# Performance work log

Measured on AMD Instinct MI355X. Metric: run time of the kernel, lower is better.

## Reference

```python
import jax, jax.numpy as jnp
import numpy as np

N = 200000          # nodes
E = 6400000         # edges
F_IN, F_HID, F_OUT = 256, 16, 3
BN_EPS = 1e-5


def setup_inputs() -> dict:
    key = jax.random.key(0)
    ks = jax.random.split(key, 8)
    x = jax.random.normal(ks[0], (N, F_IN), dtype=jnp.float32)
    edge_index = jax.random.randint(ks[1], (2, E), 0, N, dtype=jnp.int64)
    # GCNConv params (PyG: glorot weight, zero bias)
    W1 = jax.random.normal(ks[2], (F_IN, F_HID), dtype=jnp.float32) * (1.0 / np.sqrt(F_IN))
    b1 = jnp.zeros((F_HID,), dtype=jnp.float32)
    W2 = jax.random.normal(ks[3], (F_HID, F_OUT), dtype=jnp.float32) * (1.0 / np.sqrt(F_HID))
    b2 = jnp.zeros((F_OUT,), dtype=jnp.float32)
    # BatchNorm1d affine params
    gamma = jnp.ones((F_HID,), dtype=jnp.float32)
    beta = jnp.zeros((F_HID,), dtype=jnp.float32)
    return {"x": x, "W1": W1, "b1": b1, "gamma": gamma, "beta": beta,
            "W2": W2, "b2": b2, "edge_index": edge_index}


def reference(x, W1, b1, gamma, beta, W2, b2, edge_index):
    n = x.shape[0]
    self_loop = jnp.arange(n, dtype=edge_index.dtype)
    src = jnp.concatenate([edge_index[0], self_loop])  # [E+N]
    dst = jnp.concatenate([edge_index[1], self_loop])
    # symmetric normalization D^{-1/2} (A+I) D^{-1/2}
    deg = jax.ops.segment_sum(jnp.ones_like(dst, dtype=x.dtype), dst, num_segments=n)
    dinv = jax.lax.rsqrt(deg)  # deg >= 1 due to self-loops
    ew = (dinv[src] * dinv[dst])[:, None]  # [E+N, 1]

    def gcn_conv(h, W, b):
        m = h @ W                                    # transform first (small out dim)
        agg = jax.ops.segment_sum(m[src] * ew, dst, num_segments=n)
        return agg + b

    h = gcn_conv(x, W1, b1)                          # [N, 16]
    # BatchNorm1d (training-mode batch statistics, biased variance)
    mu = h.mean(axis=0)
    var = h.var(axis=0)
    h = (h - mu) * jax.lax.rsqrt(var + BN_EPS) * gamma + beta
    h = jax.nn.relu(h)
    out = gcn_conv(h, W2, b2)                        # [N, 3]
    return jax.nn.log_softmax(out, axis=1)
```

## Files before the change

kernel.cpp:

```cpp
#include <hip/hip_runtime.h>
#include <math.h>

#define F_IN 256
#define F_HID 16
#define F_OUT 3
#define BN_EPS 1e-5f
#define CAP 72

#define BUCK_SHIFT 8
#define BUCK_NODES 256
#define MAXBUCK 1024
#define CAP2 9216
#define BIN_TPB 1024
#define BIN_EPT 16
#define BIN_CHUNK (BIN_TPB * BIN_EPT)

typedef float f32x4 __attribute__((ext_vector_type(4)));
typedef short s16x8 __attribute__((ext_vector_type(8)));

__device__ __forceinline__ unsigned short bf16_rne(float f) {
    union { float f; unsigned int u; } v; v.f = f;
    unsigned int u = v.u;
    unsigned int r = (u + 0x7FFFu + ((u >> 16) & 1u)) >> 16;
    return (unsigned short)r;
}
__device__ __forceinline__ float bf16_to_f(unsigned short h) {
    union { unsigned int u; float f; } v; v.u = ((unsigned int)h) << 16;
    return v.f;
}
__device__ __forceinline__ float bflo(unsigned int w) {
    union { unsigned int u; float f; } v; v.u = w << 16; return v.f;
}
__device__ __forceinline__ float bfhi(unsigned int w) {
    union { unsigned int u; float f; } v; v.u = w & 0xFFFF0000u; return v.f;
}

__global__ void k_zero(int* __restrict__ p, int n) {
    int i = blockIdx.x * blockDim.x + threadIdx.x;
    if (i < n) p[i] = 0;
}

__global__ __launch_bounds__(BIN_TPB) void k_bin(const int* __restrict__ src,
        const int* __restrict__ dst, int* __restrict__ gcur,
        unsigned int* __restrict__ bins, int e, int nbuck) {
    __shared__ int hist[MAXBUCK];
    __shared__ int base[MAXBUCK];
    int tid = threadIdx.x;
    for (int b = tid; b < nbuck; b += BIN_TPB) hist[b] = 0;
    __syncthreads();
    int k0 = blockIdx.x * BIN_CHUNK;
    int myd[BIN_EPT], mys[BIN_EPT];
    #pragma unroll
    for (int j = 0; j < BIN_EPT; ++j) {
        int k = k0 + tid + j * BIN_TPB;
        if (k < e) {
            myd[j] = dst[k];
            mys[j] = src[k];
            atomicAdd(&hist[myd[j] >> BUCK_SHIFT], 1);
        } else {
            myd[j] = -1;
        }
    }
    __syncthreads();
    for (int b = tid; b < nbuck; b += BIN_TPB) {
        int c = hist[b];
        base[b] = (c > 0) ? atomicAdd(&gcur[b], c) : 0;
        hist[b] = 0;
    }
    __syncthreads();
    #pragma unroll
    for (int j = 0; j < BIN_EPT; ++j) {
        if (myd[j] >= 0) {
            int b = myd[j] >> BUCK_SHIFT;
            int p = atomicAdd(&hist[b], 1) + base[b];
            if (p < CAP2)
                bins[(size_t)b * CAP2 + p] =
                    ((unsigned int)mys[j] << BUCK_SHIFT) |
                    (unsigned int)(myd[j] & (BUCK_NODES - 1));
        }
    }
}

__global__ __launch_bounds__(1024) void k_regroup(const unsigned int* __restrict__ bins,
        const int* __restrict__ gcur, int* __restrict__ ssrcp,
        int* __restrict__ cnt, int n) {
    __shared__ int hist[BUCK_NODES];
    __shared__ int cur[BUCK_NODES];
    int b = blockIdx.x, tid = threadIdx.x;
    if (tid < BUCK_NODES) { hist[tid] = 0; cur[tid] = 0; }
    __syncthreads();
    int m = min(gcur[b], CAP2);
    const unsigned int* row = bins + (size_t)b * CAP2;
    for (int k = tid; k < m; k += 1024)
        atomicAdd(&hist[row[k] & (BUCK_NODES - 1)], 1);
    __syncthreads();
    if (tid < BUCK_NODES) {
        int node = b * BUCK_NODES + tid;
        if (node < n) cnt[node] = hist[tid];
    }
    for (int k = tid; k < m; k += 1024) {
        unsigned int w = row[k];
        int dl = (int)(w & (BUCK_NODES - 1));
        int p = atomicAdd(&cur[dl], 1);
        if (p < CAP)
            ssrcp[((size_t)b * BUCK_NODES + dl) * CAP + p] = (int)(w >> BUCK_SHIFT);
    }
}

__global__ __launch_bounds__(256) void k_gemm1m(
    const float* __restrict__ x, const float* __restrict__ W1,
    const int* __restrict__ cnt, unsigned int* __restrict__ msc2, int n) {
    __shared__ __align__(16) unsigned short wp[8][2][64][8];
    int tid = threadIdx.x;
    for (int idx = tid; idx < 4096; idx += 256) {
        int j = idx & 7, l = (idx >> 3) & 63, s = idx >> 9;
        int g = l >> 4, f = l & 15;
        int k = 32 * s + 4 * g + (j & 3) + ((j >> 2) << 4);
        float w = W1[k * F_HID + f];
        unsigned short hi = bf16_rne(w);
        unsigned short lo = bf16_rne(w - bf16_to_f(hi));
        wp[s][0][l][j] = hi;
        wp[s][1][l][j] = lo;
    }
    __syncthreads();
    int wid = tid >> 6, lane = tid & 63;
    int tile = blockIdx.x * 4 + wid;
    int n0 = tile * 16;
    if (n0 >= n) return;
    int g = lane >> 4, ar = lane & 15;
    const float* xr = x + (size_t)(n0 + ar) * F_IN;
    f32x4 acc = {0.f, 0.f, 0.f, 0.f};
    #pragma unroll
    for (int s = 0; s < 8; ++s) {
        float4 a0 = *(const float4*)(xr + 32 * s + 4 * g);
        float4 a1 = *(const float4*)(xr + 32 * s + 16 + 4 * g);
        float av[8] = {a0.x, a0.y, a0.z, a0.w, a1.x, a1.y, a1.z, a1.w};
        s16x8 vah, val;
        #pragma unroll
        for (int j = 0; j < 8; ++j) {
            unsigned short hi = bf16_rne(av[j]);
            unsigned short lo = bf16_rne(av[j] - bf16_to_f(hi));
            vah[j] = (short)hi;
            val[j] = (short)lo;
        }
        s16x8 bh = *(const s16x8*)&wp[s][0][lane][0];
        s16x8 bl = *(const s16x8*)&wp[s][1][lane][0];
        acc = __builtin_amdgcn_mfma_f32_16x16x32_bf16(val, bh, acc, 0, 0, 0);
        acc = __builtin_amdgcn_mfma_f32_16x16x32_bf16(vah, bl, acc, 0, 0, 0);
        acc = __builtin_amdgcn_mfma_f32_16x16x32_bf16(vah, bh, acc, 0, 0, 0);
    }
    int f = lane & 15;
    #pragma unroll
    for (int q = 0; q < 4; ++q) {
        int node = n0 + 4 * g + q;
        float di = (node < n) ? rsqrtf(1.f + (float)cnt[node]) : 0.f;
        float v = acc[q] * di;
        float vp = __shfl_xor(v, 1);
        if (((lane & 1) == 0) && node < n) {
            unsigned int pk = ((unsigned int)bf16_rne(vp) << 16) | (unsigned int)bf16_rne(v);
            msc2[(size_t)node * 8 + (f >> 1)] = pk;
        }
    }
}

__global__ __launch_bounds__(256) void k_agg1p(const unsigned int* __restrict__ msc2,
        const int* __restrict__ cnt, const int* __restrict__ ssrcp,
        const float* __restrict__ b1, float* __restrict__ h, int n) {
    int wave = (blockIdx.x * blockDim.x + threadIdx.x) >> 6;
    if (wave >= n) return;
    int lane = threadIdx.x & 63;
    int f2 = lane & 7, e8 = lane >> 3;
    int deg = cnt[wave];
    int m = min(deg, CAP);
    const int* row = ssrcp + (size_t)wave * CAP;
    int sidx[9];
    #pragma unroll
    for (int j = 0; j < 9; ++j) {
        int k = e8 + 8 * j;
        int rv = row[k];
        sidx[j] = (k < m) ? rv : wave;
    }
    unsigned int sw = msc2[(size_t)wave * 8 + f2];
    float a0 = (e8 == 0) ? bflo(sw) : 0.f;
    float a1 = (e8 == 0) ? bfhi(sw) : 0.f;
    #pragma unroll
    for (int j = 0; j < 9; ++j) {
        unsigned int w = msc2[(size_t)sidx[j] * 8 + f2];
        bool p = (e8 + 8 * j) < m;
        a0 += p ? bflo(w) : 0.f;
        a1 += p ? bfhi(w) : 0.f;
    }
    a0 += __shfl_xor(a0, 8);  a1 += __shfl_xor(a1, 8);
    a0 += __shfl_xor(a0, 16); a1 += __shfl_xor(a1, 16);
    a0 += __shfl_xor(a0, 32); a1 += __shfl_xor(a1, 32);
    if (e8 == 0) {
        float di = rsqrtf(1.f + (float)deg);
        float2 o = {di * a0 + b1[2 * f2], di * a1 + b1[2 * f2 + 1]};
        *(float2*)&h[(size_t)wave * F_HID + 2 * f2] = o;
    }
}

__global__ __launch_bounds__(256) void k_bnstats1(const float* __restrict__ h,
                                                  float* __restrict__ partial, int n) {
    __shared__ float lds[4][32];
    int i = blockIdx.x * 256 + threadIdx.x;
    float s[F_HID], s2[F_HID];
    #pragma unroll
    for (int j = 0; j < F_HID; ++j) { s[j] = 0.f; s2[j] = 0.f; }
    if (i < n) {
        const float4* a = (const float4*)(h + (size_t)i * F_HID);
        #pragma unroll
        for (int q = 0; q < 4; ++q) {
            float4 v = a[q];
            s[q*4+0] = v.x; s2[q*4+0] = v.x * v.x;
            s[q*4+1] = v.y; s2[q*4+1] = v.y * v.y;
            s[q*4+2] = v.z; s2[q*4+2] = v.z * v.z;
            s[q*4+3] = v.w; s2[q*4+3] = v.w * v.w;
        }
    }
    int lane = threadIdx.x & 63, w = threadIdx.x >> 6;
    #pragma unroll
    for (int j = 0; j < F_HID; ++j) {
        float v = s[j], u = s2[j];
        #pragma unroll
        for (int off = 32; off > 0; off >>= 1) {
            v += __shfl_xor(v, off);
            u += __shfl_xor(u, off);
        }
        if (lane == 0) { lds[w][j] = v; lds[w][F_HID + j] = u; }
    }
    __syncthreads();
    if (threadIdx.x < 32) {
        float t = lds[0][threadIdx.x] + lds[1][threadIdx.x]
                + lds[2][threadIdx.x] + lds[3][threadIdx.x];
        partial[(size_t)blockIdx.x * 32 + threadIdx.x] = t;
    }
}

__global__ __launch_bounds__(256) void k_bnstats2(const float* __restrict__ partial,
                                                  float* __restrict__ bnsum, int nb) {
    __shared__ float lds[8][32];
    int j = threadIdx.x & 31, c = threadIdx.x >> 5;
    float acc = 0.f;
    for (int b = c; b < nb; b += 8)
        acc += partial[(size_t)b * 32 + j];
    lds[c][j] = acc;
    __syncthreads();
    if (threadIdx.x < 32) {
        float t = 0.f;
        #pragma unroll
        for (int c2 = 0; c2 < 8; ++c2) t += lds[c2][threadIdx.x];
        bnsum[threadIdx.x] = t;
    }
}

__global__ void k_bn_gemm2p(const float* __restrict__ h, const int* __restrict__ cnt,
        const float* __restrict__ gamma, const float* __restrict__ beta,
        const float* __restrict__ bnsum, const float* __restrict__ W2,
        uint2* __restrict__ m2s2, int n) {
    int i = blockIdx.x * blockDim.x + threadIdx.x;
    if (i >= n) return;
    float inv_n = 1.0f / (float)n;
    float hb[F_HID];
    const float4* a = (const float4*)(h + (size_t)i * F_HID);
    #pragma unroll
    for (int q = 0; q < 4; ++q) {
        float4 v = a[q];
        float hv[4] = {v.x, v.y, v.z, v.w};
        #pragma unroll
        for (int u = 0; u < 4; ++u) {
            int j = q * 4 + u;
            float S = bnsum[j], S2 = bnsum[F_HID + j];
            float mu = S * inv_n;
            float var = fmaxf(S2 * inv_n - mu * mu, 0.f);
            float bn = (hv[u] - mu) * rsqrtf(var + BN_EPS) * gamma[j] + beta[j];
            hb[j] = fmaxf(bn, 0.f);
        }
    }
    float di = rsqrtf(1.f + (float)cnt[i]);
    float op[F_OUT];
    #pragma unroll
    for (int j = 0; j < F_OUT; ++j) {
        float acc = 0.f;
        #pragma unroll
        for (int k = 0; k < F_HID; ++k)
            acc += hb[k] * W2[k * F_OUT + j];
        op[j] = acc * di;
    }
    uint2 pk;
    pk.x = ((unsigned int)bf16_rne(op[1]) << 16) | (unsigned int)bf16_rne(op[0]);
    pk.y = (unsigned int)bf16_rne(op[2]);
    m2s2[i] = pk;
}

__global__ __launch_bounds__(256) void k_agg2p(const unsigned short* __restrict__ m2,
        const int* __restrict__ cnt, const int* __restrict__ ssrcp,
        const float* __restrict__ b2, float* __restrict__ out, int n) {
    int wave = (blockIdx.x * blockDim.x + threadIdx.x) >> 6;
    if (wave >= n) return;
    int lane = threadIdx.x & 63;
    int f = lane & 3, e16 = lane >> 2;
    int deg = cnt[wave];
    int m = min(deg, CAP);
    const int* row = ssrcp + (size_t)wave * CAP;
    int sidx[5];
    #pragma unroll
    for (int j = 0; j < 5; ++j) {
        int k = e16 + 16 * j;
        int rv = row[min(k, CAP - 1)];
        sidx[j] = (k < m) ? rv : wave;
    }
    float self = bf16_to_f(m2[(size_t)wave * 4 + f]);
    float acc = (e16 == 0) ? self : 0.f;
    #pragma unroll
    for (int j = 0; j < 5; ++j) {
        float v = bf16_to_f(m2[(size_t)sidx[j] * 4 + f]);
        acc += ((e16 + 16 * j) < m) ? v : 0.f;
    }
    acc += __shfl_xor(acc, 4);
    acc += __shfl_xor(acc, 8);
    acc += __shfl_xor(acc, 16);
    acc += __shfl_xor(acc, 32);
    float o = rsqrtf(1.f + (float)deg) * acc + ((f < 3) ? b2[f] : -1e30f);
    int base = lane & ~3;
    float o0 = __shfl(o, base + 0);
    float o1 = __shfl(o, base + 1);
    float o2 = __shfl(o, base + 2);
    float mm = fmaxf(o0, fmaxf(o1, o2));
    float lse = mm + logf(expf(o0 - mm) + expf(o1 - mm) + expf(o2 - mm));
    if (f < 3) out[(size_t)wave * 3 + f] = o - lse;
}

__global__ void k_scatterpad(const int* __restrict__ src, const int* __restrict__ dst,
                             int* __restrict__ cnt, int* __restrict__ ssrcp, int e) {
    int i = blockIdx.x * blockDim.x + threadIdx.x;
    if (i >= e) return;
    int d = dst[i];
    int pos = atomicAdd(&cnt[d], 1);
    if (pos < CAP)
        __builtin_nontemporal_store(src[i], &ssrcp[(size_t)d * CAP + pos]);
}


extern "C" void kernel_launch(void* const* d_in, const int* in_sizes, int n_in,
                              void* d_out, int out_size, void* d_ws, size_t ws_size,
                              hipStream_t stream) {
    const float* x     = (const float*)d_in[0];
    const float* W1    = (const float*)d_in[1];
    const float* b1    = (const float*)d_in[2];
    const float* gamma = (const float*)d_in[3];
    const float* beta  = (const float*)d_in[4];
    const float* W2    = (const float*)d_in[5];
    const float* b2    = (const float*)d_in[6];
    const int*   ei    = (const int*)d_in[7];

    int n = in_sizes[0] / F_IN;
    int e = in_sizes[7] / 2;
    const int* srcIdx = ei;
    const int* dstIdx = ei + e;

    int nb    = (n + 255) / 256;
    int eb    = (e + 255) / 256;
    int mb    = (n + 63) / 64;
    int wb    = (n + 3) / 4;
    int nbuck = (n + BUCK_NODES - 1) / BUCK_NODES;
    int binb  = (e + BIN_CHUNK - 1) / BIN_CHUNK;

    size_t fcnt = (size_t)26 * n + 32 + (size_t)nb * 32;
    size_t bins_cnt = (size_t)nbuck * CAP2;
    size_t union_cnt = fcnt > bins_cnt ? fcnt : bins_cnt;
    size_t bucket_need = (union_cnt + (size_t)nbuck + (size_t)n + (size_t)n * CAP) * 4;

    float* fw      = (float*)d_ws;
    unsigned int* msc2 = (unsigned int*)fw;
    float* hbuf    = fw + (size_t)8 * n;
    uint2* m2s2    = (uint2*)(fw + (size_t)24 * n);
    float* bnsum   = fw + (size_t)26 * n;
    float* partial = fw + (size_t)26 * n + 32;
    unsigned int* bins = (unsigned int*)fw;
    int* iw    = (int*)(fw + union_cnt);
    int* gcur  = iw;
    int* cnt   = iw + nbuck;
    int* ssrcp = iw + nbuck + n;

    if (ws_size >= bucket_need) {
        k_zero     <<<1, 1024, 0, stream>>>(gcur, nbuck);
        k_bin      <<<binb, BIN_TPB, 0, stream>>>(srcIdx, dstIdx, gcur, bins, e, nbuck);
        k_regroup  <<<nbuck, 1024, 0, stream>>>(bins, gcur, ssrcp, cnt, n);
        k_gemm1m   <<<mb, 256, 0, stream>>>(x, W1, cnt, msc2, n);
        k_agg1p    <<<wb, 256, 0, stream>>>(msc2, cnt, ssrcp, b1, hbuf, n);
        k_bnstats1 <<<nb, 256, 0, stream>>>(hbuf, partial, n);
        k_bnstats2 <<<1, 256, 0, stream>>>(partial, bnsum, nb);
        k_bn_gemm2p<<<nb, 256, 0, stream>>>(hbuf, cnt, gamma, beta, bnsum, W2, m2s2, n);
        k_agg2p    <<<wb, 256, 0, stream>>>((const unsigned short*)m2s2, cnt, ssrcp, b2,
                                            (float*)d_out, n);
    } else {
        int* iw2    = (int*)(fw + fcnt);
        int* cnt2   = iw2;
        int* ssrcp2 = iw2 + n;
        k_zero      <<<nb, 256, 0, stream>>>(cnt2, n);
        k_scatterpad<<<eb, 256, 0, stream>>>(srcIdx, dstIdx, cnt2, ssrcp2, e);
        k_gemm1m    <<<mb, 256, 0, stream>>>(x, W1, cnt2, msc2, n);
        k_agg1p     <<<wb, 256, 0, stream>>>(msc2, cnt2, ssrcp2, b1, hbuf, n);
        k_bnstats1  <<<nb, 256, 0, stream>>>(hbuf, partial, n);
        k_bnstats2  <<<1, 256, 0, stream>>>(partial, bnsum, nb);
        k_bn_gemm2p <<<nb, 256, 0, stream>>>(hbuf, cnt2, gamma, beta, bnsum, W2, m2s2, n);
        k_agg2p     <<<wb, 256, 0, stream>>>((const unsigned short*)m2s2, cnt2, ssrcp2, b2,
                                             (float*)d_out, n);
    }
}
```

Before: 323.5 us.

## Split first-layer messages into two feature halves and drop low-bf16 x term

The bf16 messages from the first GEMM are stored as two separate 8-feature arrays, each 16 bytes per node, instead of one 32-byte-per-node array. Aggregation runs as two launches, one per half, so each pass gathers from a smaller array that fits caches better, at the cost of reading the neighbour index lists twice. The GEMM also drops the low-part correction MFMA for x (the x-lo × W-hi term), cutting one MFMA and the conversion work per step while slightly reducing precision.

After: 346.4 us. +7.1%, slower.

```diff
diff --git a/kernel.cpp b/kernel.cpp
--- a/kernel.cpp
+++ b/kernel.cpp
@@ -109,7 +109,8 @@
 
 __global__ __launch_bounds__(256) void k_gemm1m(
     const float* __restrict__ x, const float* __restrict__ W1,
-    const int* __restrict__ cnt, unsigned int* __restrict__ msc2, int n) {
+    const int* __restrict__ cnt, unsigned int* __restrict__ mscA,
+    unsigned int* __restrict__ mscB, int n) {
     __shared__ __align__(16) unsigned short wp[8][2][64][8];
     int tid = threadIdx.x;
     for (int idx = tid; idx < 4096; idx += 256) {
@@ -135,17 +136,12 @@
         float4 a0 = *(const float4*)(xr + 32 * s + 4 * g);
         float4 a1 = *(const float4*)(xr + 32 * s + 16 + 4 * g);
         float av[8] = {a0.x, a0.y, a0.z, a0.w, a1.x, a1.y, a1.z, a1.w};
-        s16x8 vah, val;
-        #pragma unroll
-        for (int j = 0; j < 8; ++j) {
-            unsigned short hi = bf16_rne(av[j]);
-            unsigned short lo = bf16_rne(av[j] - bf16_to_f(hi));
-            vah[j] = (short)hi;
-            val[j] = (short)lo;
-        }
+        s16x8 vah;
+        #pragma unroll
+        for (int j = 0; j < 8; ++j)
+            vah[j] = (short)bf16_rne(av[j]);
         s16x8 bh = *(const s16x8*)&wp[s][0][lane][0];
         s16x8 bl = *(const s16x8*)&wp[s][1][lane][0];
-        acc = __builtin_amdgcn_mfma_f32_16x16x32_bf16(val, bh, acc, 0, 0, 0);
         acc = __builtin_amdgcn_mfma_f32_16x16x32_bf16(vah, bl, acc, 0, 0, 0);
         acc = __builtin_amdgcn_mfma_f32_16x16x32_bf16(vah, bh, acc, 0, 0, 0);
     }
@@ -158,45 +154,47 @@
         float vp = __shfl_xor(v, 1);
         if (((lane & 1) == 0) && node < n) {
             unsigned int pk = ((unsigned int)bf16_rne(vp) << 16) | (unsigned int)bf16_rne(v);
-            msc2[(size_t)node * 8 + (f >> 1)] = pk;
-        }
-    }
-}
-
-__global__ __launch_bounds__(256) void k_agg1p(const unsigned int* __restrict__ msc2,
+            if (f < 8) mscA[(size_t)node * 4 + (f >> 1)] = pk;
+            else       mscB[(size_t)node * 4 + ((f - 8) >> 1)] = pk;
+        }
+    }
+}
+
+__global__ __launch_bounds__(256) void k_agg1h(const unsigned int* __restrict__ msch,
         const int* __restrict__ cnt, const int* __restrict__ ssrcp,
-        const float* __restrict__ b1, float* __restrict__ h, int n) {
+        const float* __restrict__ b1, float* __restrict__ h, int n, int foff) {
     int wave = (blockIdx.x * blockDim.x + threadIdx.x) >> 6;
     if (wave >= n) return;
     int lane = threadIdx.x & 63;
-    int f2 = lane & 7, e8 = lane >> 3;
+    int f4 = lane & 3, e16 = lane >> 2;
     int deg = cnt[wave];
     int m = min(deg, CAP);
     const int* row = ssrcp + (size_t)wave * CAP;
-    int sidx[9];
-    #pragma unroll
-    for (int j = 0; j < 9; ++j) {
-        int k = e8 + 8 * j;
-        int rv = row[k];
+    int sidx[5];
+    #pragma unroll
+    for (int j = 0; j < 5; ++j) {
+        int k = e16 + 16 * j;
+        int rv = row[min(k, CAP - 1)];
         sidx[j] = (k < m) ? rv : wave;
     }
-    unsigned int sw = msc2[(size_t)wave * 8 + f2];
-    float a0 = (e8 == 0) ? bflo(sw) : 0.f;
-    float a1 = (e8 == 0) ? bfhi(sw) : 0.f;
-    #pragma unroll
-    for (int j = 0; j < 9; ++j) {
-        unsigned int w = msc2[(size_t)sidx[j] * 8 + f2];
-        bool p = (e8 + 8 * j) < m;
+    unsigned int sw = msch[(size_t)wave * 4 + f4];
+    float a0 = (e16 == 0) ? bflo(sw) : 0.f;
+    float a1 = (e16 == 0) ? bfhi(sw) : 0.f;
+    #pragma unroll
+    for (int j = 0; j < 5; ++j) {
+        unsigned int w = msch[(size_t)sidx[j] * 4 + f4];
+        bool p = (e16 + 16 * j) < m;
         a0 += p ? bflo(w) : 0.f;
         a1 += p ? bfhi(w) : 0.f;
     }
+    a0 += __shfl_xor(a0, 4);  a1 += __shfl_xor(a1, 4);
     a0 += __shfl_xor(a0, 8);  a1 += __shfl_xor(a1, 8);
     a0 += __shfl_xor(a0, 16); a1 += __shfl_xor(a1, 16);
     a0 += __shfl_xor(a0, 32); a1 += __shfl_xor(a1, 32);
-    if (e8 == 0) {
+    if (e16 == 0) {
         float di = rsqrtf(1.f + (float)deg);
-        float2 o = {di * a0 + b1[2 * f2], di * a1 + b1[2 * f2 + 1]};
-        *(float2*)&h[(size_t)wave * F_HID + 2 * f2] = o;
+        float2 o = {di * a0 + b1[foff + 2 * f4], di * a1 + b1[foff + 2 * f4 + 1]};
+        *(float2*)&h[(size_t)wave * F_HID + foff + 2 * f4] = o;
     }
 }
 
@@ -372,7 +370,8 @@
     size_t bucket_need = (union_cnt + (size_t)nbuck + (size_t)n + (size_t)n * CAP) * 4;
 
     float* fw      = (float*)d_ws;
-    unsigned int* msc2 = (unsigned int*)fw;
+    unsigned int* mscA = (unsigned int*)fw;
+    unsigned int* mscB = (unsigned int*)fw + (size_t)4 * n;
     float* hbuf    = fw + (size_t)8 * n;
     uint2* m2s2    = (uint2*)(fw + (size_t)24 * n);
     float* bnsum   = fw + (size_t)26 * n;
@@ -387,8 +386,9 @@
         k_zero     <<<1, 1024, 0, stream>>>(gcur, nbuck);
         k_bin      <<<binb, BIN_TPB, 0, stream>>>(srcIdx, dstIdx, gcur, bins, e, nbuck);
         k_regroup  <<<nbuck, 1024, 0, stream>>>(bins, gcur, ssrcp, cnt, n);
-        k_gemm1m   <<<mb, 256, 0, stream>>>(x, W1, cnt, msc2, n);
-        k_agg1p    <<<wb, 256, 0, stream>>>(msc2, cnt, ssrcp, b1, hbuf, n);
+        k_gemm1m   <<<mb, 256, 0, stream>>>(x, W1, cnt, mscA, mscB, n);
+        k_agg1h    <<<wb, 256, 0, stream>>>(mscA, cnt, ssrcp, b1, hbuf, n, 0);
+        k_agg1h    <<<wb, 256, 0, stream>>>(mscB, cnt, ssrcp, b1, hbuf, n, 8);
         k_bnstats1 <<<nb, 256, 0, stream>>>(hbuf, partial, n);
         k_bnstats2 <<<1, 256, 0, stream>>>(partial, bnsum, nb);
         k_bn_gemm2p<<<nb, 256, 0, stream>>>(hbuf, cnt, gamma, beta, bnsum, W2, m2s2, n);
@@ -400,8 +400,9 @@
         int* ssrcp2 = iw2 + n;
         k_zero      <<<nb, 256, 0, stream>>>(cnt2, n);
         k_scatterpad<<<eb, 256, 0, stream>>>(srcIdx, dstIdx, cnt2, ssrcp2, e);
-        k_gemm1m    <<<mb, 256, 0, stream>>>(x, W1, cnt2, msc2, n);
-        k_agg1p     <<<wb, 256, 0, stream>>>(msc2, cnt2, ssrcp2, b1, hbuf, n);
+        k_gemm1m    <<<mb, 256, 0, stream>>>(x, W1, cnt2, mscA, mscB, n);
+        k_agg1h     <<<wb, 256, 0, stream>>>(mscA, cnt2, ssrcp2, b1, hbuf, n, 0);
+        k_agg1h     <<<wb, 256, 0, stream>>>(mscB, cnt2, ssrcp2, b1, hbuf, n, 8);
         k_bnstats1  <<<nb, 256, 0, stream>>>(hbuf, partial, n);
         k_bnstats2  <<<1, 256, 0, stream>>>(partial, bnsum, nb);
         k_bn_gemm2p <<<nb, 256, 0, stream>>>(hbuf, cnt2, gamma, beta, bnsum, W2, m2s2, n);
```
